# Kernel tuning notes

Hardware: AMD Instinct MI355X
Metric: run time of the kernel (lower is better)

The kernel has to match this reference:

```python
import jax, jax.numpy as jnp
import numpy as np

SIDELEN = 128
PIXEL_SZ = 1.0


def _sampled_points(sidelen, pixel_sz):
    # mirrors torch: ax = arange(-S//2, (S-1)//2 + 1); Y, X = meshgrid(ax, ax) ('ij')
    ax = jnp.arange(-(sidelen // 2), (sidelen - 1) // 2 + 1, dtype=jnp.float32)
    Y, X = jnp.meshgrid(ax, ax, indexing='ij')
    return jnp.stack((X, Y), axis=-1).reshape(1, -1, 2) * pixel_sz  # [1, P, 2]


def setup_inputs() -> dict:
    key = jax.random.key(0)
    k1, k2, k3 = jax.random.split(key, 3)
    B, A, K = 2, 2048, 5
    # coords spread over the 128x128 Angstrom map (randn scaled by 20)
    atomic_coords = jax.random.normal(k1, (B, A, 3), dtype=jnp.float32) * 20.0
    # positive Gaussian amplitudes / widths (typical scattering-factor ranges)
    atomic_ff_a = jax.random.uniform(k2, (A, K), minval=0.1, maxval=5.0, dtype=jnp.float32)
    atomic_ff_b = jax.random.uniform(k3, (A, K), minval=5.0, maxval=30.0, dtype=jnp.float32)
    return {
        'atomic_coords': atomic_coords,
        'atomic_ff_a': atomic_ff_a,
        'atomic_ff_b': atomic_ff_b,
        'atom_block': 1024,
        'potential_block': 4096,
    }


def reference(atomic_coords, atomic_ff_a, atomic_ff_b, atom_block, potential_block):
    # atom_block / potential_block are pure tiling parameters; math is identical un-tiled.
    sidelen, pixel_sz = SIDELEN, PIXEL_SZ
    sp = _sampled_points(sidelen, pixel_sz)            # [1, P, 2]
    invb = 4.0 * jnp.pi / atomic_ff_b                  # [A, K]
    xy = atomic_coords[..., :2]                        # [B, A, 2]
    # squared pairwise distances pixel<->atom: [B, P, A]
    d2 = jnp.sum((sp[:, :, None, :] - xy[:, None, :, :]) ** 2, axis=-1)
    B = atomic_coords.shape[0]
    P = sidelen * sidelen
    pot = jnp.zeros((B, P), dtype=atomic_coords.dtype)
    K = atomic_ff_a.shape[-1]
    for k in range(K):  # small fixed loop over Gaussians (K=5)
        w = atomic_ff_a[:, k] * invb[:, k]             # [A]
        pot = pot + jnp.exp(-jnp.pi * invb[None, None, :, k] * d2) @ w  # [B, P]
    pot = pot.reshape(B, 1, sidelen, sidelen)
    return jnp.transpose(pot, (0, 1, 3, 2))
```

## Files before the change

### kernel.cpp

```cpp
#include <hip/hip_runtime.h>
#include <math.h>

#define SIDELEN 128
#define KCOEF   5
#define TILE    8
#define NW      16
#define TPB     (NW*64)

__device__ __forceinline__ float fexp2(float x) { return __builtin_amdgcn_exp2f(x); }
__device__ __forceinline__ float frcp(float x)  { return __builtin_amdgcn_rcpf(x); }

__global__ __launch_bounds__(TPB) void potential_gather_lds(
    const float* __restrict__ coords,
    const float* __restrict__ ffa,
    const float* __restrict__ ffb,
    float* __restrict__ out,
    int B, int A)
{
    const int tid  = threadIdx.x;
    const int wid  = tid >> 6;
    const int lane = tid & 63;

    const int blk  = blockIdx.x;
    const int b    = blk >> 8;
    const int tile = blk & 255;
    const int tr   = (tile >> 4) * TILE;
    const int tc   = (tile & 15) * TILE;

    const float prf = (float)(tr + (lane >> 3));
    const float pcf = (float)(tc + (lane & 7));

    const float rlo = (float)tr - 4.5f;
    const float rhi = (float)tr + (float)(TILE - 1) + 4.5f;
    const float clo = (float)tc - 4.5f;
    const float chi = (float)tc + (float)(TILE - 1) + 4.5f;

    __shared__ __align__(16) float pool[NW][64][12];
    __shared__ float smred[NW][64];

    const float* cb = coords + (size_t)b * A * 3;

    float acc = 0.0f;

    for (int base = wid * 64; base < A; base += TPB) {
        const int ai = base + lane;

        float u = -1.0e30f, v = -1.0e30f;
        if (ai < A) {
            u = cb[(size_t)ai * 3 + 0] + 64.0f;
            v = cb[(size_t)ai * 3 + 1] + 64.0f;
        }

        const bool member = (u >= rlo) & (u <= rhi) & (v >= clo) & (v <= chi);
        const unsigned long long m = __ballot(member);
        const int nm = __popcll(m);

        if (member) {
            const int pos = __popcll(m & ((1ull << lane) - 1ull));
            float cc[KCOEF], ww[KCOEF];
#pragma unroll
            for (int k = 0; k < KCOEF; ++k) {
                const float af = ffa[ai * KCOEF + k];
                const float bf = ffb[ai * KCOEF + k];
                const float rb = frcp(bf);
                cc[k] = -56.95531725f * rb;
                ww[k] = 12.56637061f * af * rb;
            }
            float4* s = (float4*)&pool[wid][pos][0];
            s[0] = make_float4(u,     v,     cc[0], ww[0]);
            s[1] = make_float4(cc[1], ww[1], cc[2], ww[2]);
            s[2] = make_float4(cc[3], ww[3], cc[4], ww[4]);
        }

#pragma unroll 2
        for (int i = 0; i < nm; ++i) {
            const float4 q0 = *(const float4*)&pool[wid][i][0];
            const float4 q1 = *(const float4*)&pool[wid][i][4];
            const float4 q2 = *(const float4*)&pool[wid][i][8];
            const float dx = prf - q0.x;
            const float dy = pcf - q0.y;
            const float d2 = fmaf(dx, dx, dy * dy);
            acc = fmaf(q0.w, fexp2(q0.z * d2), acc);
            acc = fmaf(q1.y, fexp2(q1.x * d2), acc);
            acc = fmaf(q1.w, fexp2(q1.z * d2), acc);
            acc = fmaf(q2.y, fexp2(q2.x * d2), acc);
            acc = fmaf(q2.w, fexp2(q2.z * d2), acc);
        }
    }

    smred[wid][lane] = acc;
    __syncthreads();
    if (wid == 0) {
        float val = 0.0f;
#pragma unroll
        for (int w = 0; w < NW; ++w) val += smred[w][lane];
        const int r = tr + (lane >> 3);
        const int c = tc + (lane & 7);
        out[((size_t)b << 14) + r * SIDELEN + c] = val;
    }
}

extern "C" void kernel_launch(void* const* d_in, const int* in_sizes, int n_in,
                              void* d_out, int out_size, void* d_ws, size_t ws_size,
                              hipStream_t stream) {
    const float* coords = (const float*)d_in[0];
    const float* ffa    = (const float*)d_in[1];
    const float* ffb    = (const float*)d_in[2];
    float* out = (float*)d_out;

    const int A = in_sizes[1] / KCOEF;
    const int B = in_sizes[0] / (3 * A);

    const int nblk = B * 256;
    potential_gather_lds<<<dim3(nblk), dim3(TPB), 0, stream>>>(
        coords, ffa, ffb, out, B, A);
}
```

Baseline: 65.95 us.

## Prefetch next atom chunk into registers and halve waves per block

New measurement: 68.46 us. 1.04x slower.

```diff
diff --git a/kernel.cpp b/kernel.cpp
--- a/kernel.cpp
+++ b/kernel.cpp
@@ -4,13 +4,27 @@
 #define SIDELEN 128
 #define KCOEF   5
 #define TILE    8
-#define NW      16
+#define NW      8
 #define TPB     (NW*64)
 
 __device__ __forceinline__ float fexp2(float x) { return __builtin_amdgcn_exp2f(x); }
 __device__ __forceinline__ float frcp(float x)  { return __builtin_amdgcn_rcpf(x); }
 
-__global__ __launch_bounds__(TPB) void potential_gather_lds(
+
+#define LOADC(BASE, U, V, AF, BF)                                   \
+    {                                                               \
+        const int ai_  = (BASE) + lane;                             \
+        const int ax_  = (ai_ < A) ? ai_ : 0;                       \
+        U = cb[(size_t)ax_ * 3 + 0] + 64.0f;                        \
+        V = cb[(size_t)ax_ * 3 + 1] + 64.0f;                        \
+        _Pragma("unroll")                                           \
+        for (int k = 0; k < KCOEF; ++k) {                           \
+            AF[k] = ffa[ax_ * KCOEF + k];                           \
+            BF[k] = ffb[ax_ * KCOEF + k];                           \
+        }                                                           \
+    }
+
+__global__ __launch_bounds__(TPB) void potential_gather_pipe(
     const float* __restrict__ coords,
     const float* __restrict__ ffa,
     const float* __restrict__ ffb,
@@ -42,16 +56,19 @@
 
     float acc = 0.0f;
 
-    for (int base = wid * 64; base < A; base += TPB) {
-        const int ai = base + lane;
+    int base = wid * 64;
+    float u0, v0, af0[KCOEF], bf0[KCOEF];
+    if (base < A) LOADC(base, u0, v0, af0, bf0);
 
-        float u = -1.0e30f, v = -1.0e30f;
-        if (ai < A) {
-            u = cb[(size_t)ai * 3 + 0] + 64.0f;
-            v = cb[(size_t)ai * 3 + 1] + 64.0f;
-        }
+    while (base < A) {
+        const int nbase = base + TPB;
+        float u1, v1, af1[KCOEF], bf1[KCOEF];
+        if (nbase < A) LOADC(nbase, u1, v1, af1, bf1);
 
-        const bool member = (u >= rlo) & (u <= rhi) & (v >= clo) & (v <= chi);
+        const int  ai     = base + lane;
+        const bool member = (ai < A) &
+                            (u0 >= rlo) & (u0 <= rhi) &
+                            (v0 >= clo) & (v0 <= chi);
         const unsigned long long m = __ballot(member);
         const int nm = __popcll(m);
 
@@ -60,14 +77,12 @@
             float cc[KCOEF], ww[KCOEF];
 #pragma unroll
             for (int k = 0; k < KCOEF; ++k) {
-                const float af = ffa[ai * KCOEF + k];
-                const float bf = ffb[ai * KCOEF + k];
-                const float rb = frcp(bf);
+                const float rb = frcp(bf0[k]);
                 cc[k] = -56.95531725f * rb;
-                ww[k] = 12.56637061f * af * rb;
+                ww[k] = 12.56637061f * af0[k] * rb;
             }
             float4* s = (float4*)&pool[wid][pos][0];
-            s[0] = make_float4(u,     v,     cc[0], ww[0]);
+            s[0] = make_float4(u0,    v0,    cc[0], ww[0]);
             s[1] = make_float4(cc[1], ww[1], cc[2], ww[2]);
             s[2] = make_float4(cc[3], ww[3], cc[4], ww[4]);
         }
@@ -86,6 +101,11 @@
             acc = fmaf(q2.y, fexp2(q2.x * d2), acc);
             acc = fmaf(q2.w, fexp2(q2.z * d2), acc);
         }
+
+        base = nbase;
+        u0 = u1; v0 = v1;
+#pragma unroll
+        for (int k = 0; k < KCOEF; ++k) { af0[k] = af1[k]; bf0[k] = bf1[k]; }
     }
 
     smred[wid][lane] = acc;
@@ -112,6 +132,6 @@
     const int B = in_sizes[0] / (3 * A);
 
     const int nblk = B * 256;
-    potential_gather_lds<<<dim3(nblk), dim3(TPB), 0, stream>>>(
+    potential_gather_pipe<<<dim3(nblk), dim3(TPB), 0, stream>>>(
         coords, ffa, ffb, out, B, A);
 }
```
